# Kernel optimization log

Hardware: AMD Instinct MI355X
Metric: run time of the kernel (lower is better)

The kernel has to match this reference:

```python
import jax, jax.numpy as jnp
import numpy as np
from jax import lax

N_ITER = 50  # entmax-bisect iterations (entmax library default)
DEG = 12    # neighbors per node in global item graph


def entmax_bisect(X, alpha):
    # entmax with per-row alpha, over axis=1. X: [B, L, 1], alpha: [B, 1, 1]
    d = X.shape[1]
    Xa = X * (alpha - 1.0)
    inv = 1.0 / (alpha - 1.0)
    _p = lambda z: jnp.maximum(z, 0.0) ** inv
    max_val = jnp.max(Xa, axis=1, keepdims=True)
    tau_lo = max_val - 1.0                                   # _gp(1, alpha) = 1
    tau_hi = max_val - jnp.power(1.0 / d, alpha - 1.0)       # _gp(1/d, alpha)
    f_lo = jnp.sum(_p(Xa - tau_lo), axis=1, keepdims=True) - 1.0

    def body(i, carry):
        tau_lo, dm, _ = carry
        dm = dm * 0.5
        tau_m = tau_lo + dm
        f_m = jnp.sum(_p(Xa - tau_m), axis=1, keepdims=True) - 1.0
        tau_lo = jnp.where(f_m * f_lo >= 0.0, tau_m, tau_lo)
        return (tau_lo, dm, tau_m)

    tau_lo, dm, tau_m = lax.fori_loop(0, N_ITER, body, (tau_lo, tau_hi - tau_lo, tau_lo))
    p_m = _p(Xa - tau_m)
    return p_m / jnp.sum(p_m, axis=1, keepdims=True)  # ensure_sum_one


def setup_inputs() -> dict:
    key = jax.random.key(0)
    ks = jax.random.split(key, 10)
    B, L, D, N = 1024, 50, 256, 40000
    E = N * DEG
    stdv = 1.0 / np.sqrt(D)
    u = lambda k, shape: jax.random.uniform(k, shape, jnp.float32, -stdv, stdv)

    item_emb = u(ks[0], (N, D)).at[0].set(0.0)  # padding_idx=0
    items = jax.random.randint(ks[1], (B, L), 0, N)
    inputs_seq = jax.random.randint(ks[2], (B, L), 0, N)
    alias_inputs = jax.random.randint(ks[3], (B, L), 0, L)
    target_embedding = jax.random.normal(ks[4], (B, 1, 2 * D), jnp.float32)

    # sparse global item adjacency (row-normalized, DEG neighbors per node)
    adj_rows = jnp.repeat(jnp.arange(N, dtype=jnp.int32), DEG)
    adj_cols = jax.random.randint(ks[5], (E,), 0, N, dtype=jnp.int32)
    adj_vals = jax.random.uniform(ks[6], (E,), jnp.float32) / DEG

    kp = jax.random.split(ks[7], 10)
    return {
        "items": items, "inputs_seq": inputs_seq, "alias_inputs": alias_inputs,
        "target_embedding": target_embedding, "item_emb": item_emb,
        "adj_rows": adj_rows, "adj_cols": adj_cols, "adj_vals": adj_vals,
        "wf_w": u(kp[0], (D, 2 * D)), "wf_b": u(kp[1], (D,)),
        "alphaw_w": u(kp[2], (1, D)), "alphaw_b": u(kp[3], (1,)),
        "at_w0": u(kp[4], (1, D)), "at_w1": u(kp[5], (D, D)),
        "at_w2": u(kp[6], (D, D)), "at_bias": u(kp[7], (D,)),
    }


def reference(items, inputs_seq, alias_inputs, target_embedding, item_emb,
              adj_rows, adj_cols, adj_vals, wf_w, wf_b, alphaw_w, alphaw_b,
              at_w0, at_w1, at_w2, at_bias):
    N = item_emb.shape[0]
    # GlobalItemConv (1 layer): h = (x + adj @ x) / 2 via sparse SpMM
    agg = jax.ops.segment_sum(adj_vals[:, None] * item_emb[adj_cols], adj_rows,
                              num_segments=N)
    graph_embs = (item_emb + agg) * 0.5

    hidden = graph_embs[items]                              # [B, L, D] (dropout: eval)
    target_emb = target_embedding @ wf_w.T + wf_b           # [B, 1, D]

    # get_alpha: sigmoid + 1, then masked_fill(==1 -> 1.00001)
    alpha_ent = jax.nn.sigmoid(target_emb @ alphaw_w.T + alphaw_b) + 1.0  # [B,1,1]
    alpha_ent = jnp.where(alpha_ent == 1.0, 1.00001, alpha_ent)

    # tglobal_attention
    scores = jax.nn.relu(hidden @ at_w1 + target_emb @ at_w2 + at_bias) @ at_w0.T  # [B,L,1]
    attn = entmax_bisect(scores, alpha_ent)                 # sparse softmax over L
    c = jnp.einsum('blo,bld->bod', attn, hidden)[:, 0, :]   # alpha^T @ v, squeeze -> [B,D]

    c = jax.nn.selu(c)
    return c / jnp.linalg.norm(c, axis=-1, keepdims=True)
```

## Files before the change

### kernel.cpp

```cpp
#include <hip/hip_runtime.h>
#include <hip/hip_bf16.h>
#include <math.h>

#define BB 1024
#define LL 50
#define DD 256
#define TWO_D 512
#define NN 40000
#define DEG 12
#define NITER 50

typedef __attribute__((ext_vector_type(8))) short short8;
typedef __attribute__((ext_vector_type(4))) float floatx4;

__device__ __forceinline__ float wave_sum64(float v) {
#pragma unroll
    for (int off = 32; off > 0; off >>= 1) v += __shfl_xor(v, off, 64);
    return v;
}
__device__ __forceinline__ float wave_max64(float v) {
#pragma unroll
    for (int off = 32; off > 0; off >>= 1) v = fmaxf(v, __shfl_xor(v, off, 64));
    return v;
}
__device__ __forceinline__ float bf2f(ushort u) {
    union { unsigned int i; float f; } c; c.i = ((unsigned int)u) << 16; return c.f;
}
__device__ __forceinline__ ushort f2bf(float f) {
    __hip_bfloat16 h = __float2bfloat16(f);
    return *(ushort*)&h;
}
__device__ __forceinline__ float hw_exp2(float x) { return __builtin_amdgcn_exp2f(x); }
__device__ __forceinline__ float hw_log2(float x) { return __builtin_amdgcn_logf(x); }

__global__ __launch_bounds__(256) void k_stage1(
    const float* __restrict__ emb, ushort* __restrict__ ebf,
    const int* __restrict__ items, int* __restrict__ flags,
    const float* __restrict__ wf_w, const float* __restrict__ wf_b,
    const float* __restrict__ at_w2, const float* __restrict__ at_bias,
    const float* __restrict__ aw, const float* __restrict__ ab,
    const float* __restrict__ at_w1,
    float* __restrict__ Wc, float* __restrict__ v,
    float* __restrict__ bc, float* __restrict__ c0,
    ushort* __restrict__ w1t)
{
    __shared__ float wred[4];
    __shared__ ushort s_t[4][DD];
    int bid = blockIdx.x;
    int tid = threadIdx.x;

    if (bid < 512) {
        int k = bid;
        int lane = tid & 63, wv = tid >> 6;

        float acc = 0.f;
#pragma unroll 4
        for (int d = 0; d < DD; ++d)
            acc += wf_w[d * TWO_D + k] * at_w2[d * DD + tid];
        Wc[k * DD + tid] = acc;

        float s1 = wf_w[tid * TWO_D + k] * aw[tid];
        s1 = wave_sum64(s1);
        if (lane == 0) wred[wv] = s1;
        __syncthreads();
        if (tid == 0) v[k] = wred[0] + wred[1] + wred[2] + wred[3];

        if (k < 64) {
            int k0 = k * 4;
#pragma unroll
            for (int j = 0; j < 4; ++j)
                s_t[j][tid] = f2bf(at_w1[(k0 + j) * DD + tid]);
            __syncthreads();
            ushort4 pk;
            pk.x = s_t[0][tid]; pk.y = s_t[1][tid];
            pk.z = s_t[2][tid]; pk.w = s_t[3][tid];
            *(ushort4*)(w1t + tid * DD + k0) = pk;
        }

        if (k == 0) {
            float acc2 = at_bias[tid];
#pragma unroll 4
            for (int d = 0; d < DD; ++d)
                acc2 += wf_b[d] * at_w2[d * DD + tid];
            bc[tid] = acc2;
            __syncthreads();
            float s2 = wf_b[tid] * aw[tid];
            s2 = wave_sum64(s2);
            if (lane == 0) wred[wv] = s2;
            __syncthreads();
            if (tid == 0) c0[0] = wred[0] + wred[1] + wred[2] + wred[3] + ab[0];
        }
    } else if (bid < 712) {
        int i = (bid - 512) * 256 + tid;
        flags[items[i]] = 1;
    } else {
        int i = ((bid - 712) * 256 + tid) * 4;
        float4 val = *(const float4*)(emb + i);
        ushort4 o;
        o.x = f2bf(val.x); o.y = f2bf(val.y); o.z = f2bf(val.z); o.w = f2bf(val.w);
        *(ushort4*)(ebf + i) = o;
    }
}

__global__ __launch_bounds__(256) void k_stage2(
    const ushort* __restrict__ ebf, const int* __restrict__ adj_cols,
    const float* __restrict__ adj_vals, const int* __restrict__ flags,
    ushort* __restrict__ gbf,
    const float* __restrict__ tgt, const float* __restrict__ Wc,
    const float* __restrict__ bc, const float* __restrict__ v,
    const float* __restrict__ c0, float* __restrict__ t2,
    float* __restrict__ alpha)
{
    __shared__ float x_s[4 * TWO_D];
    int bid = blockIdx.x;
    int tid = threadIdx.x;
    int wv = tid >> 6, lane = tid & 63;

    if (bid < 1024) {
        int t = bid;
        int btile = t >> 2, ntile = t & 3;
        int b0 = btile * 4, n0 = ntile * 64;
        int j = wv;
        for (int i = tid; i < 4 * TWO_D; i += 256) x_s[i] = tgt[b0 * TWO_D + i];
        __syncthreads();

        float acc = bc[n0 + lane];
        const float* xr = x_s + j * TWO_D;
#pragma unroll 8
        for (int k = 0; k < TWO_D; ++k)
            acc += xr[k] * Wc[k * DD + n0 + lane];
        t2[(b0 + j) * DD + n0 + lane] = acc;

        if (ntile == 0) {
            float s = 0.f;
#pragma unroll
            for (int i = 0; i < 8; ++i) s += xr[lane + 64 * i] * v[lane + 64 * i];
            s = wave_sum64(s);
            if (lane == 0) {
                float a = 1.f + 1.f / (1.f + expf(-(s + c0[0])));
                if (a == 1.f) a = 1.00001f;
                alpha[b0 + j] = a;
            }
        }
    } else {
        int n = (bid - 1024) * 4 + wv;
        if (flags[n] != 1) return;
        int colv = 0; float valv = 0.f;
        if (lane < DEG) { colv = adj_cols[n * DEG + lane]; valv = adj_vals[n * DEG + lane]; }
        int cols[DEG]; float vals[DEG];
#pragma unroll
        for (int k = 0; k < DEG; ++k) {
            cols[k] = __shfl(colv, k, 64);
            vals[k] = __shfl(valv, k, 64);
        }
        ushort4 s = *(const ushort4*)(ebf + (size_t)n * DD + lane * 4);
        ushort4 e[DEG];
#pragma unroll
        for (int k = 0; k < DEG; ++k)
            e[k] = *(const ushort4*)(ebf + (size_t)cols[k] * DD + lane * 4);
        float a0 = bf2f(s.x), a1 = bf2f(s.y), a2 = bf2f(s.z), a3 = bf2f(s.w);
#pragma unroll
        for (int k = 0; k < DEG; ++k) {
            float vv = vals[k];
            a0 += vv * bf2f(e[k].x); a1 += vv * bf2f(e[k].y);
            a2 += vv * bf2f(e[k].z); a3 += vv * bf2f(e[k].w);
        }
        ushort4 o;
        o.x = f2bf(0.5f * a0); o.y = f2bf(0.5f * a1);
        o.z = f2bf(0.5f * a2); o.w = f2bf(0.5f * a3);
        *(ushort4*)(gbf + (size_t)n * DD + lane * 4) = o;
    }
}

__global__ __launch_bounds__(256, 2) void k_scores_mfma(
    const int* __restrict__ items, const ushort* __restrict__ gbf,
    const ushort* __restrict__ w1t, const float* __restrict__ t2,
    const float* __restrict__ at_w0, float* __restrict__ scores)
{
    __shared__ __align__(16) ushort sA[128 * 72];
    __shared__ __align__(16) ushort sB[256 * 72];
    __shared__ float sred[128][4];
    __shared__ int s_items[128];
    int tid = threadIdx.x;
    int blk = blockIdx.x;
    int lane = tid & 63, wv = tid >> 6;
    int cn = lane & 15, q = lane >> 4;
    int n0 = wv * 64;

    if (tid < 128) s_items[tid] = items[blk * 128 + tid];
    __syncthreads();

    floatx4 acc[8][4];
#pragma unroll
    for (int mt = 0; mt < 8; ++mt)
#pragma unroll
        for (int nt = 0; nt < 4; ++nt)
            acc[mt][nt] = (floatx4){0.f, 0.f, 0.f, 0.f};

#pragma unroll 1
    for (int kc = 0; kc < 4; ++kc) {
#pragma unroll
        for (int it = 0; it < 4; ++it) {
            int i = tid + it * 256;
            int row = i >> 3, seg = i & 7;
            *(uint4*)(sA + row * 72 + seg * 8) =
                *(const uint4*)(gbf + (size_t)s_items[row] * DD + kc * 64 + seg * 8);
        }
#pragma unroll
        for (int it = 0; it < 8; ++it) {
            int i = tid + it * 256;
            int n = i >> 3, seg = i & 7;
            *(uint4*)(sB + n * 72 + seg * 8) =
                *(const uint4*)(w1t + n * DD + kc * 64 + seg * 8);
        }
        __syncthreads();
#pragma unroll
        for (int ks = 0; ks < 2; ++ks) {
            short8 af[8], bfr[4];
#pragma unroll
            for (int mt = 0; mt < 8; ++mt)
                af[mt] = *(const short8*)(sA + (mt * 16 + cn) * 72 + ks * 32 + q * 8);
#pragma unroll
            for (int nt = 0; nt < 4; ++nt)
                bfr[nt] = *(const short8*)(sB + (n0 + nt * 16 + cn) * 72 + ks * 32 + q * 8);
#pragma unroll
            for (int mt = 0; mt < 8; ++mt)
#pragma unroll
                for (int nt = 0; nt < 4; ++nt)
                    acc[mt][nt] = __builtin_amdgcn_mfma_f32_16x16x32_bf16(
                        af[mt], bfr[nt], acc[mt][nt], 0, 0, 0);
        }
        __syncthreads();
    }

    float w0v[4];
#pragma unroll
    for (int nt = 0; nt < 4; ++nt) w0v[nt] = at_w0[n0 + nt * 16 + cn];
#pragma unroll
    for (int mt = 0; mt < 8; ++mt) {
#pragma unroll
        for (int r = 0; r < 4; ++r) {
            int row_in = q * 4 + r;
            int row = mt * 16 + row_in;
            int b = (blk * 128 + row) / LL;
            const float* t2b = t2 + b * DD;
            float p = 0.f;
#pragma unroll
            for (int nt = 0; nt < 4; ++nt) {
                int col = n0 + nt * 16 + cn;
                float vv = acc[mt][nt][r] + t2b[col];
                p += fmaxf(vv, 0.f) * w0v[nt];
            }
            p += __shfl_xor(p, 1, 64);
            p += __shfl_xor(p, 2, 64);
            p += __shfl_xor(p, 4, 64);
            p += __shfl_xor(p, 8, 64);
            if (cn == 0) sred[row][wv] = p;
        }
    }
    __syncthreads();
    if (tid < 128)
        scores[blk * 128 + tid] = sred[tid][0] + sred[tid][1] + sred[tid][2] + sred[tid][3];
}

__device__ __forceinline__ float pw(float z, float invv) {
    return hw_exp2(invv * hw_log2(z));
}

__global__ __launch_bounds__(256) void k_entmax_out(
    const float* __restrict__ scores, const float* __restrict__ alpha,
    const int* __restrict__ items, const ushort* __restrict__ gbf,
    float* __restrict__ out)
{
    __shared__ float attn_s[LL];
    __shared__ int s_it[LL];
    __shared__ float red[4];
    int b = blockIdx.x;
    int tid = threadIdx.x;

    if (tid >= 192 && tid < 192 + LL) s_it[tid - 192] = items[b * LL + (tid - 192)];

    if (tid < 64) {
        int l = tid;
        float a = alpha[b];
        float am1 = a - 1.f;
        float invv = 1.f / am1;
        float x = (l < LL) ? scores[b * LL + l] : -__builtin_inff();
        float Xa = x * am1;

        float mx = wave_max64(Xa);
        float tau_lo = mx - 1.f;
        float tau_hi = mx - hw_exp2(am1 * hw_log2(1.f / (float)LL));

        float f_lo = wave_sum64(pw(fmaxf(Xa - tau_lo, 0.f), invv)) - 1.f;

        float dm = tau_hi - tau_lo;
        float tau_m = tau_lo;
#pragma unroll 1
        for (int it = 0; it < NITER; ++it) {
            dm *= 0.5f;
            tau_m = tau_lo + dm;
            if (tau_m == tau_lo) break;
            float f_m = wave_sum64(pw(fmaxf(Xa - tau_m, 0.f), invv)) - 1.f;
            if (f_m * f_lo >= 0.f) tau_lo = tau_m;
        }
        float pm = pw(fmaxf(Xa - tau_m, 0.f), invv);
        float s = wave_sum64(pm);
        if (l < LL) attn_s[l] = pm / s;
    }
    __syncthreads();

    int d = tid;
    float c = 0.f;
#pragma unroll
    for (int l = 0; l < LL; ++l)
        c += attn_s[l] * bf2f(gbf[(size_t)s_it[l] * DD + d]);

    const float SC = 1.0507009873554805f;
    const float AL = 1.6732632423543772f;
    c = SC * (c > 0.f ? c : AL * expm1f(c));

    float ss = wave_sum64(c * c);
    int wv = tid >> 6, lane = tid & 63;
    if (lane == 0) red[wv] = ss;
    __syncthreads();
    float tot = red[0] + red[1] + red[2] + red[3];
    out[b * DD + d] = c / sqrtf(tot);
}

extern "C" void kernel_launch(void* const* d_in, const int* in_sizes, int n_in,
                              void* d_out, int out_size, void* d_ws, size_t ws_size,
                              hipStream_t stream) {
    const int*   items     = (const int*)  d_in[0];
    const float* tgt       = (const float*)d_in[3];
    const float* item_emb  = (const float*)d_in[4];
    const int*   adj_cols  = (const int*)  d_in[6];
    const float* adj_vals  = (const float*)d_in[7];
    const float* wf_w      = (const float*)d_in[8];
    const float* wf_b      = (const float*)d_in[9];
    const float* alphaw_w  = (const float*)d_in[10];
    const float* alphaw_b  = (const float*)d_in[11];
    const float* at_w0     = (const float*)d_in[12];
    const float* at_w1     = (const float*)d_in[13];
    const float* at_w2     = (const float*)d_in[14];
    const float* at_bias   = (const float*)d_in[15];

    const size_t SZ_TAB = (size_t)NN * DD * sizeof(ushort);
    char* ws = (char*)d_ws;
    ushort* gbf = (ushort*)ws;   ws += SZ_TAB;
    ushort* ebf = (ushort*)ws;   ws += SZ_TAB;
    ushort* w1t = (ushort*)ws;   ws += (size_t)DD * DD * sizeof(ushort);
    int*   flags = (int*)ws;     ws += (size_t)NN * sizeof(int);
    float* Wc     = (float*)ws;  ws += (size_t)TWO_D * DD * sizeof(float);
    float* bcv    = (float*)ws;  ws += (size_t)DD * sizeof(float);
    float* vv     = (float*)ws;  ws += (size_t)TWO_D * sizeof(float);
    float* c0v    = (float*)ws;  ws += 16 * sizeof(float);
    float* t2     = (float*)ws;  ws += (size_t)BB * DD * sizeof(float);
    float* alpha  = (float*)ws;  ws += ((size_t)BB + 32) * sizeof(float);
    float* scores = (float*)ws;  ws += (size_t)BB * LL * sizeof(float);
    float* out    = (float*)d_out;

    k_stage1<<<10712, 256, 0, stream>>>(item_emb, ebf, items, flags,
                                        wf_w, wf_b, at_w2, at_bias,
                                        alphaw_w, alphaw_b, at_w1,
                                        Wc, vv, bcv, c0v, w1t);
    k_stage2<<<11024, 256, 0, stream>>>(ebf, adj_cols, adj_vals, flags, gbf,
                                        tgt, Wc, bcv, vv, c0v, t2, alpha);
    k_scores_mfma<<<(BB * LL) / 128, 256, 0, stream>>>(items, gbf, w1t, t2, at_w0, scores);
    k_entmax_out<<<BB, 256, 0, stream>>>(scores, alpha, items, gbf, out);
}
```

Baseline: 204.3 us.

## Drop bf16 copy of embedding table; gather fp32 rows directly in SpMM

Removes the stage that converted the full 40000x256 fp32 embedding table to bf16, and has the sparse aggregation gather fp32 rows straight from the input table. Only rows flagged as used are touched, so the full-table read and write pass goes away, though each gather now moves twice the bytes per row. The weight-fusion GEMV in stage1 also caches the wf_w column in shared memory and splits the reduction into 8 accumulators, so it does fewer strided global loads and has more independent work in flight.

```diff
diff --git a/kernel.cpp b/kernel.cpp
--- a/kernel.cpp
+++ b/kernel.cpp
@@ -34,7 +34,6 @@
 __device__ __forceinline__ float hw_log2(float x) { return __builtin_amdgcn_logf(x); }
 
 __global__ __launch_bounds__(256) void k_stage1(
-    const float* __restrict__ emb, ushort* __restrict__ ebf,
     const int* __restrict__ items, int* __restrict__ flags,
     const float* __restrict__ wf_w, const float* __restrict__ wf_b,
     const float* __restrict__ at_w2, const float* __restrict__ at_bias,
@@ -44,6 +43,7 @@
     float* __restrict__ bc, float* __restrict__ c0,
     ushort* __restrict__ w1t)
 {
+    __shared__ float wcol[DD];
     __shared__ float wred[4];
     __shared__ ushort s_t[4][DD];
     int bid = blockIdx.x;
@@ -53,13 +53,22 @@
         int k = bid;
         int lane = tid & 63, wv = tid >> 6;
 
-        float acc = 0.f;
+        wcol[tid] = wf_w[tid * TWO_D + k];
+        __syncthreads();
+
+        float a[8];
+#pragma unroll
+        for (int j = 0; j < 8; ++j) a[j] = 0.f;
 #pragma unroll 4
-        for (int d = 0; d < DD; ++d)
-            acc += wf_w[d * TWO_D + k] * at_w2[d * DD + tid];
-        Wc[k * DD + tid] = acc;
-
-        float s1 = wf_w[tid * TWO_D + k] * aw[tid];
+        for (int d = 0; d < DD; d += 8) {
+#pragma unroll
+            for (int j = 0; j < 8; ++j)
+                a[j] += wcol[d + j] * at_w2[(d + j) * DD + tid];
+        }
+        Wc[k * DD + tid] = ((a[0] + a[1]) + (a[2] + a[3]))
+                         + ((a[4] + a[5]) + (a[6] + a[7]));
+
+        float s1 = wcol[tid] * aw[tid];
         s1 = wave_sum64(s1);
         if (lane == 0) wred[wv] = s1;
         __syncthreads();
@@ -78,32 +87,34 @@
         }
 
         if (k == 0) {
-            float acc2 = at_bias[tid];
+            __syncthreads();
+            wcol[tid] = wf_b[tid];
+            __syncthreads();
+            float b[8];
+#pragma unroll
+            for (int j = 0; j < 8; ++j) b[j] = 0.f;
 #pragma unroll 4
-            for (int d = 0; d < DD; ++d)
-                acc2 += wf_b[d] * at_w2[d * DD + tid];
-            bc[tid] = acc2;
-            __syncthreads();
-            float s2 = wf_b[tid] * aw[tid];
+            for (int d = 0; d < DD; d += 8) {
+#pragma unroll
+                for (int j = 0; j < 8; ++j)
+                    b[j] += wcol[d + j] * at_w2[(d + j) * DD + tid];
+            }
+            bc[tid] = at_bias[tid] + ((b[0] + b[1]) + (b[2] + b[3]))
+                                   + ((b[4] + b[5]) + (b[6] + b[7]));
+            float s2 = wcol[tid] * aw[tid];
             s2 = wave_sum64(s2);
             if (lane == 0) wred[wv] = s2;
             __syncthreads();
             if (tid == 0) c0[0] = wred[0] + wred[1] + wred[2] + wred[3] + ab[0];
         }
-    } else if (bid < 712) {
+    } else {
         int i = (bid - 512) * 256 + tid;
         flags[items[i]] = 1;
-    } else {
-        int i = ((bid - 712) * 256 + tid) * 4;
-        float4 val = *(const float4*)(emb + i);
-        ushort4 o;
-        o.x = f2bf(val.x); o.y = f2bf(val.y); o.z = f2bf(val.z); o.w = f2bf(val.w);
-        *(ushort4*)(ebf + i) = o;
     }
 }
 
 __global__ __launch_bounds__(256) void k_stage2(
-    const ushort* __restrict__ ebf, const int* __restrict__ adj_cols,
+    const float* __restrict__ emb, const int* __restrict__ adj_cols,
     const float* __restrict__ adj_vals, const int* __restrict__ flags,
     ushort* __restrict__ gbf,
     const float* __restrict__ tgt, const float* __restrict__ Wc,
@@ -153,17 +164,17 @@
             cols[k] = __shfl(colv, k, 64);
             vals[k] = __shfl(valv, k, 64);
         }
-        ushort4 s = *(const ushort4*)(ebf + (size_t)n * DD + lane * 4);
-        ushort4 e[DEG];
+        float4 s = *(const float4*)(emb + (size_t)n * DD + lane * 4);
+        float4 e[DEG];
 #pragma unroll
         for (int k = 0; k < DEG; ++k)
-            e[k] = *(const ushort4*)(ebf + (size_t)cols[k] * DD + lane * 4);
-        float a0 = bf2f(s.x), a1 = bf2f(s.y), a2 = bf2f(s.z), a3 = bf2f(s.w);
+            e[k] = *(const float4*)(emb + (size_t)cols[k] * DD + lane * 4);
+        float a0 = s.x, a1 = s.y, a2 = s.z, a3 = s.w;
 #pragma unroll
         for (int k = 0; k < DEG; ++k) {
             float vv = vals[k];
-            a0 += vv * bf2f(e[k].x); a1 += vv * bf2f(e[k].y);
-            a2 += vv * bf2f(e[k].z); a3 += vv * bf2f(e[k].w);
+            a0 += vv * e[k].x; a1 += vv * e[k].y;
+            a2 += vv * e[k].z; a3 += vv * e[k].w;
         }
         ushort4 o;
         o.x = f2bf(0.5f * a0); o.y = f2bf(0.5f * a1);
@@ -348,7 +359,6 @@
     const size_t SZ_TAB = (size_t)NN * DD * sizeof(ushort);
     char* ws = (char*)d_ws;
     ushort* gbf = (ushort*)ws;   ws += SZ_TAB;
-    ushort* ebf = (ushort*)ws;   ws += SZ_TAB;
     ushort* w1t = (ushort*)ws;   ws += (size_t)DD * DD * sizeof(ushort);
     int*   flags = (int*)ws;     ws += (size_t)NN * sizeof(int);
     float* Wc     = (float*)ws;  ws += (size_t)TWO_D * DD * sizeof(float);
@@ -360,11 +370,11 @@
     float* scores = (float*)ws;  ws += (size_t)BB * LL * sizeof(float);
     float* out    = (float*)d_out;
 
-    k_stage1<<<10712, 256, 0, stream>>>(item_emb, ebf, items, flags,
-                                        wf_w, wf_b, at_w2, at_bias,
-                                        alphaw_w, alphaw_b, at_w1,
-                                        Wc, vv, bcv, c0v, w1t);
-    k_stage2<<<11024, 256, 0, stream>>>(ebf, adj_cols, adj_vals, flags, gbf,
+    k_stage1<<<712, 256, 0, stream>>>(items, flags,
+                                      wf_w, wf_b, at_w2, at_bias,
+                                      alphaw_w, alphaw_b, at_w1,
+                                      Wc, vv, bcv, c0v, w1t);
+    k_stage2<<<11024, 256, 0, stream>>>(item_emb, adj_cols, adj_vals, flags, gbf,
                                         tgt, Wc, bcv, vv, c0v, t2, alpha);
     k_scores_mfma<<<(BB * LL) / 128, 256, 0, stream>>>(items, gbf, w1t, t2, at_w0, scores);
     k_entmax_out<<<BB, 256, 0, stream>>>(scores, alpha, items, gbf, out);
```

New measurement: 200.7 us. No clear change (-1.8%).
